# Kernel optimization log

Measured on AMD Instinct MI355X. Metric: run time of the kernel, lower is better.

Reference implementation:

```python
import jax, jax.numpy as jnp
import numpy as np
from jax.scipy.special import logsumexp

B, DK, N, M = 16, 512, 1024, 1024
SINKHORN_ITERS = 5
EPS = 1e-8


def setup_inputs() -> dict:
    key = jax.random.key(0)
    k1, k2, k3, k4, k5 = jax.random.split(key, 5)
    return {
        "src_embedding": jax.random.normal(k1, (B, DK, N), dtype=jnp.float32),
        "tgt_embedding": jax.random.normal(k2, (B, DK, M), dtype=jnp.float32),
        "src": jax.random.normal(k3, (B, 3, N), dtype=jnp.float32),
        "tgt": jax.random.normal(k4, (B, 3, M), dtype=jnp.float32),
        # temperature must be positive; uniform in [0.05, 1.0)
        "temperature": jax.random.uniform(k5, (B,), dtype=jnp.float32, minval=0.05, maxval=1.0),
    }


def sinkhorn(scores, n_iters):
    # ZeroPad2d((0,1,0,1)): pad one slack row and one slack column with zeros
    scores = jnp.pad(scores, ((0, 0), (0, 1), (0, 1)))
    for _ in range(n_iters):
        # row normalization (all rows except slack row)
        top = scores[:, :-1, :] - logsumexp(scores[:, :-1, :], axis=2, keepdims=True)
        scores = jnp.concatenate([top, scores[:, -1:, :]], axis=1)
        # column normalization (all cols except slack col)
        left = scores[:, :, :-1] - logsumexp(scores[:, :, :-1], axis=1, keepdims=True)
        scores = jnp.concatenate([left, scores[:, :, -1:]], axis=2)
    return scores[:, :-1, :-1]


def reference(src_embedding, tgt_embedding, src, tgt, temperature):
    b, d_k, n = src_embedding.shape
    # [B, N, M] similarity scores
    dists = jnp.einsum('bdn,bdm->bnm', src_embedding, tgt_embedding) / jnp.sqrt(jnp.float32(d_k))
    affinity = dists / temperature[:, None, None]
    log_perm = sinkhorn(affinity, SINKHORN_ITERS)
    perm = jnp.exp(log_perm)                                             # [B,N,M]
    perm_norm = perm / (jnp.sum(perm, axis=2, keepdims=True) + EPS)      # [B,N,M]
    # soft correspondence: weighted_tgt[b,:,i] = sum_j perm_norm[b,i,j] * tgt[b,:,j]
    weighted_tgt = jnp.einsum('bdm,bnm->bdn', tgt, perm_norm)            # [B,3,N]
    weights = jnp.sum(perm, axis=-1, keepdims=True)                      # [B,N,1]
    weights_norm = weights / (jnp.sum(weights, axis=1, keepdims=True) + EPS)
    weights_norm = jnp.swapaxes(weights_norm, 1, 2)                      # [B,1,N]
    src_centroid = jnp.sum(src * weights_norm, axis=2, keepdims=True)    # [B,3,1]
    tgt_centroid = jnp.sum(weighted_tgt * weights_norm, axis=2, keepdims=True)
    src_centered = src - src_centroid
    corr_centered = (weighted_tgt - tgt_centroid) * weights_norm
    # weighted cross-covariance, batched 3x3
    H = jnp.einsum('bin,bjn->bij', src_centered, corr_centered)          # [B,3,3]
    # batched Procrustes via SVD (torch.svd: H = u diag(s) v^T; jnp: H = u diag(s) vh)
    u, s, vh = jnp.linalg.svd(H)
    v = jnp.swapaxes(vh, 1, 2)
    ut = jnp.swapaxes(u, 1, 2)
    r = jnp.matmul(v, ut)
    r_det = jnp.linalg.det(r)                                            # [B]
    diag = jnp.stack([jnp.ones_like(r_det), jnp.ones_like(r_det), r_det], axis=-1)  # [B,3]
    R = jnp.matmul(v * diag[:, None, :], ut)                             # [B,3,3]
    t = (jnp.matmul(-R, src_centroid) + tgt_centroid).reshape(b, 3)
    return R, t, perm_norm
```

## Files before the change

### kernel.cpp

```cpp
#include <hip/hip_runtime.h>
#include <math.h>

#define BB 16
#define NN 1024
#define MM 1024
#define DKK 512
#define RBLK 16
#define NRB  (NN/RBLK)
#define LSTR 1032

typedef short short8 __attribute__((ext_vector_type(8)));
typedef float f32x4 __attribute__((ext_vector_type(4)));

__device__ float g_u[BB*NN];
__device__ float g_v[BB*MM];
__device__ float g_w[BB*NN];
__device__ float g_wt[BB*3*NN];
__device__ float g_pm[BB*NRB*MM];
__device__ float g_ps[BB*NRB*MM];
__device__ __attribute__((aligned(16))) unsigned short gAh[BB*NN*DKK];
__device__ __attribute__((aligned(16))) unsigned short gAl[BB*NN*DKK];
__device__ __attribute__((aligned(16))) unsigned short gBh[BB*MM*DKK];
__device__ __attribute__((aligned(16))) unsigned short gBl[BB*MM*DKK];

__global__ __launch_bounds__(256) void zero_v_kernel() {
    int i = blockIdx.x*256 + threadIdx.x;
    if (i < BB*MM) g_v[i] = 0.0f;
}

__device__ __forceinline__ unsigned int bf16_rne(float x){
    unsigned int u = __float_as_uint(x);
    return (u + 0x7fffu + ((u>>16)&1u)) >> 16;
}

__device__ __forceinline__ void gl_lds(const void* g, void* l){
    __builtin_amdgcn_global_load_lds(
        (const __attribute__((address_space(1))) unsigned int*)g,
        (__attribute__((address_space(3))) unsigned int*)l, 16, 0, 0);
}

__global__ __launch_bounds__(256) void convert_split(const float* __restrict__ A,
                                                     const float* __restrict__ Bm) {
    int z = blockIdx.z;
    int which = z >> 4;
    int b = z & 15;
    const float* X = which ? Bm : A;
    unsigned short* Hh = which ? gBh : gAh;
    unsigned short* Hl = which ? gBl : gAl;
    int d0 = blockIdx.y * 64;
    int i0 = blockIdx.x * 64;
    __shared__ float T[64*65];
    const float* Xb = X + ((size_t)b*DKK + d0)*NN + i0;
    int t = threadIdx.x;
#pragma unroll
    for (int it=0; it<4; ++it){
        int lin = t + 256*it;
        int d = lin >> 4;
        int i4 = lin & 15;
        float4 v = *(const float4*)(Xb + (size_t)d*NN + i4*4);
        T[(i4*4+0)*65 + d] = v.x;
        T[(i4*4+1)*65 + d] = v.y;
        T[(i4*4+2)*65 + d] = v.z;
        T[(i4*4+3)*65 + d] = v.w;
    }
    __syncthreads();
    size_t obase = ((size_t)b*NN + i0)*DKK + d0;
#pragma unroll
    for (int it=0; it<2; ++it){
        int c = t + 256*it;
        int i = c >> 3;
        int p = c & 7;
        unsigned int hw[4], lw[4];
#pragma unroll
        for (int j=0;j<4;j++){
            float x0 = T[i*65 + p*8 + 2*j];
            float x1 = T[i*65 + p*8 + 2*j+1];
            unsigned int h0 = bf16_rne(x0);
            unsigned int h1 = bf16_rne(x1);
            float hf0 = __uint_as_float(h0<<16);
            float hf1 = __uint_as_float(h1<<16);
            unsigned int l0 = bf16_rne(x0 - hf0);
            unsigned int l1 = bf16_rne(x1 - hf1);
            hw[j] = h0 | (h1<<16);
            lw[j] = l0 | (l1<<16);
        }
        int pw = (p & 4) | ((p + (i>>1)) & 3);
        size_t eo = obase + (size_t)i*DKK + pw*8;
        uint4 hv; hv.x=hw[0]; hv.y=hw[1]; hv.z=hw[2]; hv.w=hw[3];
        uint4 lv; lv.x=lw[0]; lv.y=lw[1]; lv.z=lw[2]; lv.w=lw[3];
        *(uint4*)(Hh + eo) = hv;
        *(uint4*)(Hl + eo) = lv;
    }
}

__global__ __launch_bounds__(512,2) void gemm_mfma(const float* __restrict__ temp,
                                                   float* __restrict__ C) {
    int id   = blockIdx.x;
    int xcd  = id & 7;
    int slot = id >> 3;
    int b    = xcd*2 + (slot >> 4);
    int sub  = slot & 15;
    int i0   = (sub >> 2) << 8;
    int j0   = (sub & 3) << 8;
    __shared__ __attribute__((aligned(16))) char lds[131072];
    int t = threadIdx.x;
    int lane = t & 63, w = t >> 6;
    int wr = w >> 2, wc = w & 3;

    int rql = lane >> 2, cl = lane & 3;
    unsigned eoff = (unsigned)(b * (NN*DKK*2));
    unsigned offA = eoff + (unsigned)((i0 + w*32 + rql)*1024) + (unsigned)(cl*16);
    unsigned offB = eoff + (unsigned)((j0 + w*32 + rql)*1024) + (unsigned)(cl*16);
    int dq0 = w*2048;

    const char* pAh = (const char*)gAh;
    const char* pAl = (const char*)gAl;
    const char* pBh = (const char*)gBh;
    const char* pBl = (const char*)gBl;

    f32x4 acc[32];
#pragma unroll
    for (int q=0;q<32;q++) acc[q] = (f32x4){0.f,0.f,0.f,0.f};

    int fslot = ((lane>>4) + ((lane&15)>>1)) & 3;
    int faoff = (wr*128 + (lane&15))*64 + fslot*16;
    int fboff = (wc*64  + (lane&15))*64 + fslot*16;

    gl_lds(pAh + offA,          lds + 0      + dq0);
    gl_lds(pAh + offA + 16384,  lds + 0      + dq0 + 1024);
    gl_lds(pBh + offB,          lds + 65536  + dq0);
    gl_lds(pBh + offB + 16384,  lds + 65536  + dq0 + 1024);
    gl_lds(pAl + offA,          lds + 32768  + dq0);
    gl_lds(pAl + offA + 16384,  lds + 32768  + dq0 + 1024);
    gl_lds(pBl + offB,          lds + 98304  + dq0);
    gl_lds(pBl + offB + 16384,  lds + 98304  + dq0 + 1024);

    short8 ah[8], bh[4], al[8], bl[4];

    for (int ks=0; ks<16; ++ks){
        int par = (ks & 1) << 14;
        int nxt = 16384 - par;

        asm volatile("s_waitcnt vmcnt(2)" ::: "memory");
        __builtin_amdgcn_s_barrier();
        __builtin_amdgcn_sched_barrier(0);
        {
            const char* fa  = lds + par + faoff;
            const char* fb  = lds + 65536 + par + fboff;
            const char* fal = lds + 32768 + par + faoff;
#pragma unroll
            for (int mf=0;mf<8;mf++) ah[mf] = *(const short8*)(fa + mf*1024);
#pragma unroll
            for (int nf=0;nf<4;nf++) bh[nf] = *(const short8*)(fb + nf*1024);
#pragma unroll
            for (int mf=0;mf<8;mf++) al[mf] = *(const short8*)(fal + mf*1024);
        }
        if (ks < 15){
            offA += 64; offB += 64;
            gl_lds(pAh + offA,         lds + 0     + nxt + dq0);
            gl_lds(pAh + offA + 16384, lds + 0     + nxt + dq0 + 1024);
            gl_lds(pBh + offB,         lds + 65536 + nxt + dq0);
            gl_lds(pBh + offB + 16384, lds + 65536 + nxt + dq0 + 1024);
            gl_lds(pAl + offA,         lds + 32768 + nxt + dq0);
            gl_lds(pAl + offA + 16384, lds + 32768 + nxt + dq0 + 1024);
        }
        __builtin_amdgcn_sched_barrier(0);
        __builtin_amdgcn_s_setprio(1);
#pragma unroll
        for (int nf=0;nf<4;nf++)
#pragma unroll
            for (int mf=0;mf<8;mf++)
                acc[mf*4+nf] = __builtin_amdgcn_mfma_f32_16x16x32_bf16(ah[mf], bh[nf], acc[mf*4+nf], 0,0,0);
#pragma unroll
        for (int nf=0;nf<4;nf++)
#pragma unroll
            for (int mf=0;mf<8;mf++)
                acc[mf*4+nf] = __builtin_amdgcn_mfma_f32_16x16x32_bf16(al[mf], bh[nf], acc[mf*4+nf], 0,0,0);
        __builtin_amdgcn_s_setprio(0);
        __builtin_amdgcn_sched_barrier(0);

        if (ks < 15) asm volatile("s_waitcnt vmcnt(6)" ::: "memory");
        else         asm volatile("s_waitcnt vmcnt(0)" ::: "memory");
        __builtin_amdgcn_s_barrier();
        __builtin_amdgcn_sched_barrier(0);
        {
            const char* fbl = lds + 98304 + par + fboff;
#pragma unroll
            for (int nf=0;nf<4;nf++) bl[nf] = *(const short8*)(fbl + nf*1024);
        }
        if (ks < 15){
            gl_lds(pBl + offB,         lds + 98304 + nxt + dq0);
            gl_lds(pBl + offB + 16384, lds + 98304 + nxt + dq0 + 1024);
        }
        __builtin_amdgcn_sched_barrier(0);
        __builtin_amdgcn_s_setprio(1);
#pragma unroll
        for (int nf=0;nf<4;nf++)
#pragma unroll
            for (int mf=0;mf<8;mf++)
                acc[mf*4+nf] = __builtin_amdgcn_mfma_f32_16x16x32_bf16(ah[mf], bl[nf], acc[mf*4+nf], 0,0,0);
        __builtin_amdgcn_s_setprio(0);
        __builtin_amdgcn_sched_barrier(0);
    }

    float scale = 1.0f/(22.62741699796952f * temp[b]);
    float* Cb = C + ((size_t)b<<20);
    int r0c = i0 + wr*128 + ((lane>>4)<<2);
    int c0c = j0 + wc*64 + (lane&15);
#pragma unroll
    for (int mf=0;mf<8;mf++){
#pragma unroll
        for (int r2=0;r2<4;r2++){
            float* rowp = Cb + (size_t)(r0c + mf*16 + r2)*MM + c0c;
#pragma unroll
            for (int nf=0;nf<4;nf++)
                rowp[nf*16] = acc[mf*4+nf][r2]*scale;
        }
    }
}

__global__ __launch_bounds__(256) void sink_iter(const float* __restrict__ S) {
    int b   = blockIdx.y;
    int rb  = blockIdx.x;
    int row0 = rb*RBLK;
    int t = threadIdx.x;
    __shared__ float Ls[RBLK*LSTR];
    __shared__ float v_l[1024];
    __shared__ float u_l[RBLK];

    float4 v4 = *(const float4*)(g_v + (b<<10) + t*4);
    *(float4*)(v_l + t*4) = v4;

    const float* Sb = S + ((size_t)b*NN + row0)*MM;
#pragma unroll
    for (int rr=0; rr<RBLK; ++rr){
        float4 s4 = *(const float4*)(Sb + (size_t)rr*MM + t*4);
        s4.x -= v4.x; s4.y -= v4.y; s4.z -= v4.z; s4.w -= v4.w;
        *(float4*)(&Ls[rr*LSTR + t*4]) = s4;
    }
    __syncthreads();

    {
        int r = t >> 4, c = t & 15;
        const float* Lr = &Ls[r*LSTR + c];
        float m = -INFINITY;
#pragma unroll
        for (int k=0;k<64;k++) m = fmaxf(m, Lr[16*k]);
#pragma unroll
        for (int off=1; off<16; off<<=1) m = fmaxf(m, __shfl_xor(m, off));
        m = fmaxf(m, 0.0f);
        float s = 0.0f;
#pragma unroll
        for (int k=0;k<64;k++) s += __expf(Lr[16*k] - m);
#pragma unroll
        for (int off=1; off<16; off<<=1) s += __shfl_xor(s, off);
        s += __expf(-m);
        float u = m + __logf(s);
        if (c==0){ u_l[r] = u; g_u[b*NN + row0 + r] = u; }
    }
    __syncthreads();

    float mm[4], ss[4];
#pragma unroll
    for (int q=0;q<4;q++){ mm[q]=-INFINITY; ss[q]=0.f; }
#pragma unroll
    for (int r=0;r<RBLK;++r){
        float ur = u_l[r];
        const float* Lr = &Ls[r*LSTR];
#pragma unroll
        for (int q=0;q<4;q++)
            mm[q] = fmaxf(mm[q], Lr[t + 256*q] - ur);
    }
#pragma unroll
    for (int r=0;r<RBLK;++r){
        float ur = u_l[r];
        const float* Lr = &Ls[r*LSTR];
#pragma unroll
        for (int q=0;q<4;q++)
            ss[q] += __expf(Lr[t + 256*q] - ur - mm[q]);
    }
    size_t pbase = ((size_t)(b*NRB + rb) << 10) + t;
#pragma unroll
    for (int q=0;q<4;q++){
        g_pm[pbase + 256*q] = mm[q] + v_l[t + 256*q];
        g_ps[pbase + 256*q] = ss[q];
    }
}

__global__ __launch_bounds__(64) void col_lse_combine() {
    int idx = blockIdx.x*64 + threadIdx.x;
    int b = idx >> 10; int j = idx & (MM-1);
    size_t base = ((size_t)(b*NRB) << 10) + j;
    float m[8], s[8];
#pragma unroll
    for (int k=0;k<8;k++){ m[k] = -INFINITY; s[k] = 0.0f; }
    for (int c=0;c<NRB;c+=8){
#pragma unroll
        for (int k=0;k<8;k++){
            float om = g_pm[base + ((size_t)(c+k)<<10)];
            float os = g_ps[base + ((size_t)(c+k)<<10)];
            float nm = fmaxf(m[k], om);
            s[k] = s[k]*__expf(m[k]-nm) + os*__expf(om-nm);
            m[k] = nm;
        }
    }
#pragma unroll
    for (int st=1; st<8; st<<=1){
#pragma unroll
        for (int k=0;k<8;k+=2*st){
            float nm = fmaxf(m[k], m[k+st]);
            s[k] = s[k]*__expf(m[k]-nm) + s[k+st]*__expf(m[k+st]-nm);
            m[k] = nm;
        }
    }
    float nm = fmaxf(m[0], 0.0f);
    float Sx = s[0]*__expf(m[0]-nm) + __expf(-nm);
    g_v[idx] = nm + __logf(Sx);
}

__global__ __launch_bounds__(256) void finalize_rows(float* __restrict__ S,
                                                     const float* __restrict__ tgt) {
    int row  = blockIdx.x*4 + (threadIdx.x>>6);
    int lane = threadIdx.x & 63;
    int b = row >> 10;
    int i = row & (NN-1);
    float ui = g_u[row];
    float4* srow = (float4*)(S + (size_t)row*MM);
    const float4* vb = (const float4*)(g_v + (b<<10));
    const float4* t0 = (const float4*)(tgt + (size_t)b*3*MM);
    const float4* t1 = (const float4*)(tgt + (size_t)b*3*MM + MM);
    const float4* t2 = (const float4*)(tgt + (size_t)b*3*MM + 2*MM);
    float p[16];
    float rs=0.f, a0=0.f, a1=0.f, a2=0.f;
#pragma unroll
    for (int k=0;k<4;k++){
        float4 s4 = srow[lane + 64*k];
        float4 v4 = vb[lane + 64*k];
        p[4*k+0] = __expf(s4.x - ui - v4.x);
        p[4*k+1] = __expf(s4.y - ui - v4.y);
        p[4*k+2] = __expf(s4.z - ui - v4.z);
        p[4*k+3] = __expf(s4.w - ui - v4.w);
        rs += p[4*k+0]+p[4*k+1]+p[4*k+2]+p[4*k+3];
        float4 w0 = t0[lane + 64*k];
        float4 w1 = t1[lane + 64*k];
        float4 w2 = t2[lane + 64*k];
        a0 += p[4*k+0]*w0.x + p[4*k+1]*w0.y + p[4*k+2]*w0.z + p[4*k+3]*w0.w;
        a1 += p[4*k+0]*w1.x + p[4*k+1]*w1.y + p[4*k+2]*w1.z + p[4*k+3]*w1.w;
        a2 += p[4*k+0]*w2.x + p[4*k+1]*w2.y + p[4*k+2]*w2.z + p[4*k+3]*w2.w;
    }
    for (int off=32; off; off>>=1){
        rs += __shfl_xor(rs, off);
        a0 += __shfl_xor(a0, off);
        a1 += __shfl_xor(a1, off);
        a2 += __shfl_xor(a2, off);
    }
    float inv = 1.0f/(rs + 1e-8f);
#pragma unroll
    for (int k=0;k<4;k++){
        srow[lane + 64*k] = make_float4(p[4*k+0]*inv, p[4*k+1]*inv, p[4*k+2]*inv, p[4*k+3]*inv);
    }
    if (lane==0){
        g_w[row] = rs;
        g_wt[(b*3+0)*NN + i] = a0*inv;
        g_wt[(b*3+1)*NN + i] = a1*inv;
        g_wt[(b*3+2)*NN + i] = a2*inv;
    }
}

__global__ __launch_bounds__(256) void procrustes(const float* __restrict__ src,
                                                  float* __restrict__ out) {
    int b = blockIdx.x;
    int t = threadIdx.x;
    int lane = t & 63, w = t >> 6;
    __shared__ float part[4][16];
    const float* wrow = g_w + b*NN;
    const float* sb  = src  + (size_t)b*3*NN;
    const float* wtb = g_wt + (size_t)b*3*NN;

    float wv[4], sv[3][4], tv3[3][4];
#pragma unroll
    for (int k=0;k<4;k++){
        int i = t + 256*k;
        wv[k] = wrow[i];
#pragma unroll
        for (int c=0;c<3;c++){
            sv[c][k]  = sb[c*NN+i];
            tv3[c][k] = wtb[c*NN+i];
        }
    }

    auto block_reduce = [&](float* v, int nv){
        for (int jx=0;jx<nv;jx++){
            float x = v[jx];
            for (int off=32;off;off>>=1) x += __shfl_xor(x, off);
            if (lane==0) part[w][jx] = x;
        }
        __syncthreads();
        for (int jx=0;jx<nv;jx++)
            v[jx] = part[0][jx]+part[1][jx]+part[2][jx]+part[3][jx];
        __syncthreads();
    };

    float W = wv[0]+wv[1]+wv[2]+wv[3];
    block_reduce(&W, 1);
    float winv = 1.0f/(W + 1e-8f);
    float wn[4];
#pragma unroll
    for (int k=0;k<4;k++) wn[k] = wv[k]*winv;

    float a[6];
#pragma unroll
    for (int c=0;c<3;c++){
        float p1=0.f,p2=0.f;
#pragma unroll
        for (int k=0;k<4;k++){ p1 += sv[c][k]*wn[k]; p2 += tv3[c][k]*wn[k]; }
        a[c]=p1; a[3+c]=p2;
    }
    block_reduce(a, 6);
    float sc[3], tc[3];
#pragma unroll
    for (int c=0;c<3;c++){ sc[c]=a[c]; tc[c]=a[3+c]; }

    float H[9];
#pragma unroll
    for (int c=0;c<3;c++)
#pragma unroll
        for (int d=0;d<3;d++){
            float p=0.f;
#pragma unroll
            for (int k=0;k<4;k++)
                p += (sv[c][k]-sc[c]) * ((tv3[d][k]-tc[d])*wn[k]);
            H[c*3+d]=p;
        }
    block_reduce(H, 9);

    if (t==0){
        double Hd[3][3];
        for (int r2=0;r2<3;r2++) for (int c2=0;c2<3;c2++) Hd[r2][c2]=H[r2*3+c2];
        double K[3][3];
        for (int i2=0;i2<3;i2++)
            for (int j2=0;j2<3;j2++){
                double acc=0;
                for (int r2=0;r2<3;r2++) acc += Hd[r2][i2]*Hd[r2][j2];
                K[i2][j2]=acc;
            }
        double V[3][3]={{1,0,0},{0,1,0},{0,0,1}};
        const int PQ[3][2]={{0,1},{0,2},{1,2}};
        for (int sweep=0; sweep<30; ++sweep){
            double off = fabs(K[0][1])+fabs(K[0][2])+fabs(K[1][2]);
            if (off < 1e-26) break;
            for (int pi=0; pi<3; ++pi){
                int p = PQ[pi][0], q = PQ[pi][1];
                double apq = K[p][q];
                if (fabs(apq) < 1e-300) continue;
                double tau = (K[q][q]-K[p][p])/(2.0*apq);
                double tt  = (tau>=0.0?1.0:-1.0)/(fabs(tau)+sqrt(1.0+tau*tau));
                double c   = 1.0/sqrt(1.0+tt*tt);
                double s   = tt*c;
                double Kpp=K[p][p], Kqq=K[q][q];
                K[p][p] = Kpp - tt*apq;
                K[q][q] = Kqq + tt*apq;
                K[p][q] = 0.0; K[q][p] = 0.0;
                int r2 = 3-p-q;
                double Krp=K[r2][p], Krq=K[r2][q];
                K[r2][p] = c*Krp - s*Krq; K[p][r2]=K[r2][p];
                K[r2][q] = s*Krp + c*Krq; K[q][r2]=K[r2][q];
                for (int rr=0; rr<3; ++rr){
                    double vp=V[rr][p], vq=V[rr][q];
                    V[rr][p] = c*vp - s*vq;
                    V[rr][q] = s*vp + c*vq;
                }
            }
        }
        double lam[3]={K[0][0],K[1][1],K[2][2]};
        int o0=0,o1=1,o2=2,tmp;
        if (lam[o0]<lam[o1]){tmp=o0;o0=o1;o1=tmp;}
        if (lam[o0]<lam[o2]){tmp=o0;o0=o2;o2=tmp;}
        if (lam[o1]<lam[o2]){tmp=o1;o1=o2;o2=tmp;}
        int ord[3]={o0,o1,o2};
        double Vs[3][3], U[3][3];
        for (int k=0;k<3;k++)
            for (int r2=0;r2<3;r2++) Vs[r2][k]=V[r2][ord[k]];
        for (int k=0;k<3;k++){
            double ux = Hd[0][0]*Vs[0][k] + Hd[0][1]*Vs[1][k] + Hd[0][2]*Vs[2][k];
            double uy = Hd[1][0]*Vs[0][k] + Hd[1][1]*Vs[1][k] + Hd[1][2]*Vs[2][k];
            double uz = Hd[2][0]*Vs[0][k] + Hd[2][1]*Vs[1][k] + Hd[2][2]*Vs[2][k];
            double n = sqrt(ux*ux+uy*uy+uz*uz);
            if (n > 1e-30){ U[0][k]=ux/n; U[1][k]=uy/n; U[2][k]=uz/n; }
            else {
                double cx = U[1][0]*U[2][1]-U[2][0]*U[1][1];
                double cy = U[2][0]*U[0][1]-U[0][0]*U[2][1];
                double cz = U[0][0]*U[1][1]-U[1][0]*U[0][1];
                U[0][k]=cx; U[1][k]=cy; U[2][k]=cz;
            }
        }
        double rm[3][3];
        for (int i2=0;i2<3;i2++)
            for (int j2=0;j2<3;j2++)
                rm[i2][j2] = Vs[i2][0]*U[j2][0] + Vs[i2][1]*U[j2][1] + Vs[i2][2]*U[j2][2];
        double det = rm[0][0]*(rm[1][1]*rm[2][2]-rm[1][2]*rm[2][1])
                   - rm[0][1]*(rm[1][0]*rm[2][2]-rm[1][2]*rm[2][0])
                   + rm[0][2]*(rm[1][0]*rm[2][1]-rm[1][1]*rm[2][0]);
        double R[3][3];
        for (int i2=0;i2<3;i2++)
            for (int j2=0;j2<3;j2++)
                R[i2][j2] = Vs[i2][0]*U[j2][0] + Vs[i2][1]*U[j2][1] + det*Vs[i2][2]*U[j2][2];
        double tvv[3];
        for (int i2=0;i2<3;i2++)
            tvv[i2] = -(R[i2][0]*sc[0]+R[i2][1]*sc[1]+R[i2][2]*sc[2]) + tc[i2];
        for (int i2=0;i2<3;i2++)
            for (int j2=0;j2<3;j2++)
                out[b*9 + i2*3 + j2] = (float)R[i2][j2];
        for (int i2=0;i2<3;i2++)
            out[144 + b*3 + i2] = (float)tvv[i2];
    }
}

extern "C" void kernel_launch(void* const* d_in, const int* in_sizes, int n_in,
                              void* d_out, int out_size, void* d_ws, size_t ws_size,
                              hipStream_t stream) {
    const float* src_emb = (const float*)d_in[0];
    const float* tgt_emb = (const float*)d_in[1];
    const float* src     = (const float*)d_in[2];
    const float* tgt     = (const float*)d_in[3];
    const float* temp    = (const float*)d_in[4];
    float* out = (float*)d_out;
    float* S = out + 192;

    hipLaunchKernelGGL(zero_v_kernel, dim3(64), dim3(256), 0, stream);
    hipLaunchKernelGGL(convert_split, dim3(16,8,32), dim3(256), 0, stream, src_emb, tgt_emb);
    hipLaunchKernelGGL(gemm_mfma, dim3(256), dim3(512), 0, stream, temp, S);
    for (int it=0; it<5; ++it){
        hipLaunchKernelGGL(sink_iter, dim3(NRB,BB), dim3(256), 0, stream, S);
        hipLaunchKernelGGL(col_lse_combine, dim3(256), dim3(64), 0, stream);
    }
    hipLaunchKernelGGL(finalize_rows, dim3(4096), dim3(256), 0, stream, S, tgt);
    hipLaunchKernelGGL(procrustes, dim3(16), dim3(256), 0, stream, src, out);
}
```

Before: 336.0 us.

## Split GEMM k-step into six interleaved LDS-read/MFMA phases with finer barriers

Restructures the split-bf16 GEMM inner loop into six smaller phases, each loading half the A fragments (or B-low fragments) from LDS and then issuing 16 MFMAs. Global-to-LDS prefetches are spread across the phases with adjusted vmcnt waits. The aim is to cut register pressure (al shrinks from 8 to 4 fragments) and to overlap LDS reads with MFMA work in a ping-pong style. In exchange it adds more barriers and explicit lgkmcnt waits, which may serialize work, and the changed vmcnt counts risk reading stale data if they are miscounted.

```diff
diff --git a/kernel.cpp b/kernel.cpp
--- a/kernel.cpp
+++ b/kernel.cpp
@@ -135,47 +135,59 @@
     gl_lds(pBl + offB,          lds + 98304  + dq0);
     gl_lds(pBl + offB + 16384,  lds + 98304  + dq0 + 1024);
 
-    short8 ah[8], bh[4], al[8], bl[4];
+    short8 ah[8], bh[4], al[4], bl[4];
 
     for (int ks=0; ks<16; ++ks){
         int par = (ks & 1) << 14;
         int nxt = 16384 - par;
-
-        asm volatile("s_waitcnt vmcnt(2)" ::: "memory");
+        const char* fa  = lds + par + faoff;
+        const char* fb  = lds + 65536 + par + fboff;
+        const char* fal = lds + 32768 + par + faoff;
+        const char* fbl = lds + 98304 + par + fboff;
+
+        asm volatile("s_waitcnt vmcnt(4)" ::: "memory");
         __builtin_amdgcn_s_barrier();
         __builtin_amdgcn_sched_barrier(0);
-        {
-            const char* fa  = lds + par + faoff;
-            const char* fb  = lds + 65536 + par + fboff;
-            const char* fal = lds + 32768 + par + faoff;
-#pragma unroll
-            for (int mf=0;mf<8;mf++) ah[mf] = *(const short8*)(fa + mf*1024);
-#pragma unroll
-            for (int nf=0;nf<4;nf++) bh[nf] = *(const short8*)(fb + nf*1024);
-#pragma unroll
-            for (int mf=0;mf<8;mf++) al[mf] = *(const short8*)(fal + mf*1024);
-        }
+#pragma unroll
+        for (int mf=0;mf<4;mf++) ah[mf] = *(const short8*)(fa + mf*1024);
+#pragma unroll
+        for (int nf=0;nf<4;nf++) bh[nf] = *(const short8*)(fb + nf*1024);
         if (ks < 15){
             offA += 64; offB += 64;
             gl_lds(pAh + offA,         lds + 0     + nxt + dq0);
             gl_lds(pAh + offA + 16384, lds + 0     + nxt + dq0 + 1024);
             gl_lds(pBh + offB,         lds + 65536 + nxt + dq0);
             gl_lds(pBh + offB + 16384, lds + 65536 + nxt + dq0 + 1024);
+        }
+        asm volatile("s_waitcnt lgkmcnt(0)" ::: "memory");
+        __builtin_amdgcn_sched_barrier(0);
+        __builtin_amdgcn_s_setprio(1);
+#pragma unroll
+        for (int nf=0;nf<4;nf++)
+#pragma unroll
+            for (int mf=0;mf<4;mf++)
+                acc[mf*4+nf] = __builtin_amdgcn_mfma_f32_16x16x32_bf16(ah[mf], bh[nf], acc[mf*4+nf], 0,0,0);
+        __builtin_amdgcn_s_setprio(0);
+        __builtin_amdgcn_sched_barrier(0);
+
+        if (ks < 15) asm volatile("s_waitcnt vmcnt(6)" ::: "memory");
+        else         asm volatile("s_waitcnt vmcnt(2)" ::: "memory");
+        __builtin_amdgcn_s_barrier();
+        __builtin_amdgcn_sched_barrier(0);
+#pragma unroll
+        for (int mf=0;mf<4;mf++) ah[4+mf] = *(const short8*)(fa + (4+mf)*1024);
+        if (ks < 15){
             gl_lds(pAl + offA,         lds + 32768 + nxt + dq0);
             gl_lds(pAl + offA + 16384, lds + 32768 + nxt + dq0 + 1024);
         }
+        asm volatile("s_waitcnt lgkmcnt(0)" ::: "memory");
         __builtin_amdgcn_sched_barrier(0);
         __builtin_amdgcn_s_setprio(1);
 #pragma unroll
         for (int nf=0;nf<4;nf++)
 #pragma unroll
-            for (int mf=0;mf<8;mf++)
-                acc[mf*4+nf] = __builtin_amdgcn_mfma_f32_16x16x32_bf16(ah[mf], bh[nf], acc[mf*4+nf], 0,0,0);
-#pragma unroll
-        for (int nf=0;nf<4;nf++)
-#pragma unroll
-            for (int mf=0;mf<8;mf++)
-                acc[mf*4+nf] = __builtin_amdgcn_mfma_f32_16x16x32_bf16(al[mf], bh[nf], acc[mf*4+nf], 0,0,0);
+            for (int mf=0;mf<4;mf++)
+                acc[(4+mf)*4+nf] = __builtin_amdgcn_mfma_f32_16x16x32_bf16(ah[4+mf], bh[nf], acc[(4+mf)*4+nf], 0,0,0);
         __builtin_amdgcn_s_setprio(0);
         __builtin_amdgcn_sched_barrier(0);
 
@@ -183,22 +195,61 @@
         else         asm volatile("s_waitcnt vmcnt(0)" ::: "memory");
         __builtin_amdgcn_s_barrier();
         __builtin_amdgcn_sched_barrier(0);
-        {
-            const char* fbl = lds + 98304 + par + fboff;
-#pragma unroll
-            for (int nf=0;nf<4;nf++) bl[nf] = *(const short8*)(fbl + nf*1024);
-        }
+#pragma unroll
+        for (int mf=0;mf<4;mf++) al[mf] = *(const short8*)(fal + mf*1024);
         if (ks < 15){
             gl_lds(pBl + offB,         lds + 98304 + nxt + dq0);
             gl_lds(pBl + offB + 16384, lds + 98304 + nxt + dq0 + 1024);
         }
+        asm volatile("s_waitcnt lgkmcnt(0)" ::: "memory");
         __builtin_amdgcn_sched_barrier(0);
         __builtin_amdgcn_s_setprio(1);
 #pragma unroll
         for (int nf=0;nf<4;nf++)
 #pragma unroll
-            for (int mf=0;mf<8;mf++)
+            for (int mf=0;mf<4;mf++)
+                acc[mf*4+nf] = __builtin_amdgcn_mfma_f32_16x16x32_bf16(al[mf], bh[nf], acc[mf*4+nf], 0,0,0);
+        __builtin_amdgcn_s_setprio(0);
+        __builtin_amdgcn_sched_barrier(0);
+
+        __builtin_amdgcn_s_barrier();
+        __builtin_amdgcn_sched_barrier(0);
+#pragma unroll
+        for (int mf=0;mf<4;mf++) al[mf] = *(const short8*)(fal + (4+mf)*1024);
+        asm volatile("s_waitcnt lgkmcnt(0)" ::: "memory");
+        __builtin_amdgcn_sched_barrier(0);
+        __builtin_amdgcn_s_setprio(1);
+#pragma unroll
+        for (int nf=0;nf<4;nf++)
+#pragma unroll
+            for (int mf=0;mf<4;mf++)
+                acc[(4+mf)*4+nf] = __builtin_amdgcn_mfma_f32_16x16x32_bf16(al[mf], bh[nf], acc[(4+mf)*4+nf], 0,0,0);
+        __builtin_amdgcn_s_setprio(0);
+        __builtin_amdgcn_sched_barrier(0);
+
+        __builtin_amdgcn_s_barrier();
+        __builtin_amdgcn_sched_barrier(0);
+#pragma unroll
+        for (int nf=0;nf<4;nf++) bl[nf] = *(const short8*)(fbl + nf*1024);
+        asm volatile("s_waitcnt lgkmcnt(0)" ::: "memory");
+        __builtin_amdgcn_sched_barrier(0);
+        __builtin_amdgcn_s_setprio(1);
+#pragma unroll
+        for (int nf=0;nf<4;nf++)
+#pragma unroll
+            for (int mf=0;mf<4;mf++)
                 acc[mf*4+nf] = __builtin_amdgcn_mfma_f32_16x16x32_bf16(ah[mf], bl[nf], acc[mf*4+nf], 0,0,0);
+        __builtin_amdgcn_s_setprio(0);
+        __builtin_amdgcn_sched_barrier(0);
+
+        __builtin_amdgcn_s_barrier();
+        __builtin_amdgcn_sched_barrier(0);
+        __builtin_amdgcn_s_setprio(1);
+#pragma unroll
+        for (int nf=0;nf<4;nf++)
+#pragma unroll
+            for (int mf=0;mf<4;mf++)
+                acc[(4+mf)*4+nf] = __builtin_amdgcn_mfma_f32_16x16x32_bf16(ah[4+mf], bl[nf], acc[(4+mf)*4+nf], 0,0,0);
         __builtin_amdgcn_s_setprio(0);
         __builtin_amdgcn_sched_barrier(0);
     }
```

Result: no change. 339.6 us (+1.1%).
